# Kernel optimization log

Measured on AMD Instinct MI355X. Metric: run time of the kernel, lower is better.

The kernel has to match this reference:

```python
import jax, jax.numpy as jnp
import numpy as np

# Fixed per-step coefficients from the module __init__ (K = 16 steps)
_H = jnp.array([-0.73437643, 3.319645, 2.1290164, 3.6901689, 3.302721, 3.2154958,
                2.9151256, 3.1718695, 3.1084518, 2.6179547, 2.235003, 1.2864777,
                0.52327204, -0.08344932, -1.8249638, 3.0859442], dtype=jnp.float32)
_D = jnp.array([3.3848417, -0.07072583, 3.691287, 3.3074934, 3.2120926, 2.9196491,
                3.1727686, 3.1054153, 2.621943, 2.2355895, 1.2878408, 0.52468026,
                0.12632068, 0.14482783, 0.3153498, 0.13054803], dtype=jnp.float32)
_T = jnp.array([3.1538513, -1.0211663, 1.3714716, 1.0718397, 1.0049332, 0.68078244,
                1.0151638, 0.8858697, 0.4037103, 0.01490025, -0.90781677, -1.6859558,
                -1.9241625, -2.0441303, 0.279356, 0.1315174], dtype=jnp.float32)


@jax.custom_vjp
def spike(v_scaled):
    # Heaviside forward with surrogate gradient (matches SpikeFunction)
    return (v_scaled > 0).astype(v_scaled.dtype)

def _spike_fwd(v_scaled):
    return spike(v_scaled), v_scaled

def _spike_bwd(v_scaled, g):
    surrogate = jnp.maximum(1.0 - jnp.abs(v_scaled), 0.0)
    return (g * surrogate,)

spike.defvjp(_spike_fwd, _spike_bwd)


def setup_inputs() -> dict:
    key = jax.random.key(0)
    x = jax.random.normal(key, (16, 4096, 1024), dtype=jnp.float32)
    return {"x": x}


def reference(x) -> jnp.ndarray:
    zeros = jnp.zeros_like(x)

    def step(carry, hdt):
        v, z, out = carry
        h_t, d_t, T_t = hdt
        v = v - z * h_t
        v_scaled = (v - T_t) / (jnp.abs(v) + 1.0)
        z = spike(v_scaled)
        out = out + z * d_t
        return (v, z, out), None

    (_, _, out), _ = jax.lax.scan(step, (x, zeros, zeros), (_H, _D, _T))
    return out
```

## Files before the change

kernel.cpp:

```cpp
#include <hip/hip_runtime.h>


typedef float f32x4 __attribute__((ext_vector_type(4)));

__device__ __constant__ const float kH[16] = {
    -0.73437643f, 3.319645f,   2.1290164f,  3.6901689f,
    3.302721f,    3.2154958f,  2.9151256f,  3.1718695f,
    3.1084518f,   2.6179547f,  2.235003f,   1.2864777f,
    0.52327204f, -0.08344932f, -1.8249638f, 3.0859442f};

__device__ __constant__ const float kD[16] = {
    3.3848417f, -0.07072583f, 3.691287f,   3.3074934f,
    3.2120926f,  2.9196491f,  3.1727686f,  3.1054153f,
    2.621943f,   2.2355895f,  1.2878408f,  0.52468026f,
    0.12632068f, 0.14482783f, 0.3153498f,  0.13054803f};

__device__ __constant__ const float kT[16] = {
    3.1538513f, -1.0211663f,  1.3714716f,  1.0718397f,
    1.0049332f,  0.68078244f, 1.0151638f,  0.8858697f,
    0.4037103f,  0.01490025f, -0.90781677f, -1.6859558f,
    -1.9241625f, -2.0441303f, 0.279356f,   0.1315174f};

__device__ __forceinline__ float spike_chain(float v) {
    float z = (v > kT[0]) ? 1.0f : 0.0f;
    float out = z * kD[0];
#pragma unroll
    for (int t = 1; t < 16; ++t) {
        v = fmaf(-z, kH[t], v);
        z = (v > kT[t]) ? 1.0f : 0.0f;
        out = fmaf(z, kD[t], out);
    }
    return out;
}

__device__ __forceinline__ f32x4 spike4(f32x4 v) {
    f32x4 o;
    o.x = spike_chain(v.x);
    o.y = spike_chain(v.y);
    o.z = spike_chain(v.z);
    o.w = spike_chain(v.w);
    return o;
}

__global__ __launch_bounds__(256) void spike_kernel(const f32x4* __restrict__ x,
                                                    f32x4* __restrict__ out,
                                                    int n4) {
    const int T = gridDim.x * blockDim.x;
    int i = blockIdx.x * blockDim.x + threadIdx.x;

    for (; i + 3 * T < n4; i += 4 * T) {
        f32x4 a = x[i];
        f32x4 b = x[i + T];
        f32x4 c = x[i + 2 * T];
        f32x4 d = x[i + 3 * T];
        f32x4 ra = spike4(a);
        f32x4 rb = spike4(b);
        f32x4 rc = spike4(c);
        f32x4 rd = spike4(d);
        __builtin_nontemporal_store(ra, &out[i]);
        __builtin_nontemporal_store(rb, &out[i + T]);
        __builtin_nontemporal_store(rc, &out[i + 2 * T]);
        __builtin_nontemporal_store(rd, &out[i + 3 * T]);
    }
    for (; i < n4; i += T) {
        f32x4 r = spike4(x[i]);
        __builtin_nontemporal_store(r, &out[i]);
    }
}

extern "C" void kernel_launch(void* const* d_in, const int* in_sizes, int n_in,
                              void* d_out, int out_size, void* d_ws, size_t ws_size,
                              hipStream_t stream) {
    const float* x = (const float*)d_in[0];
    float* out = (float*)d_out;
    int n = in_sizes[0];
    int n4 = n >> 2;

    const int block = 256;
    int grid = (n4 + 4 * block - 1) / (4 * block);

    spike_kernel<<<grid, block, 0, stream>>>(
        (const f32x4*)x, (f32x4*)out, n4);
}
```

Before: 97.50 us.

## Replace spike compare-select with packed FMA clamp step function

Computes the spike indicator as clamp(v*BIG - T*BIG) using v_pk_fma_f32 with the clamp modifier, so each step becomes three packed FMAs over pairs of elements instead of a compare plus select plus scalar FMAs. The fixed-size path drops the loop and tail checks, and a generic fallback kernel handles other sizes. The clamp trick differs from an exact Heaviside when v is within about 1/BIG of the threshold, where it gives a fractional spike value, and that error can propagate through later steps.

```diff
diff --git a/kernel.cpp b/kernel.cpp
--- a/kernel.cpp
+++ b/kernel.cpp
@@ -1,25 +1,92 @@
 #include <hip/hip_runtime.h>
 
 
+typedef float f32x2 __attribute__((ext_vector_type(2)));
 typedef float f32x4 __attribute__((ext_vector_type(4)));
 
-__device__ __constant__ const float kH[16] = {
+static constexpr float kBIG = 1099511627776.0f;
+
+static constexpr float kH[16] = {
     -0.73437643f, 3.319645f,   2.1290164f,  3.6901689f,
     3.302721f,    3.2154958f,  2.9151256f,  3.1718695f,
     3.1084518f,   2.6179547f,  2.235003f,   1.2864777f,
     0.52327204f, -0.08344932f, -1.8249638f, 3.0859442f};
 
-__device__ __constant__ const float kD[16] = {
+static constexpr float kD[16] = {
     3.3848417f, -0.07072583f, 3.691287f,   3.3074934f,
     3.2120926f,  2.9196491f,  3.1727686f,  3.1054153f,
     2.621943f,   2.2355895f,  1.2878408f,  0.52468026f,
     0.12632068f, 0.14482783f, 0.3153498f,  0.13054803f};
 
-__device__ __constant__ const float kT[16] = {
+static constexpr float kT[16] = {
     3.1538513f, -1.0211663f,  1.3714716f,  1.0718397f,
     1.0049332f,  0.68078244f, 1.0151638f,  0.8858697f,
     0.4037103f,  0.01490025f, -0.90781677f, -1.6859558f,
     -1.9241625f, -2.0441303f, 0.279356f,   0.1315174f};
+
+__device__ __forceinline__ f32x2 pk_fma(f32x2 a, f32x2 b, f32x2 c) {
+    f32x2 d;
+    asm("v_pk_fma_f32 %0, %1, %2, %3" : "=v"(d) : "v"(a), "v"(b), "v"(c));
+    return d;
+}
+
+__device__ __forceinline__ f32x2 pk_fma_clamp(f32x2 a, f32x2 b, f32x2 c) {
+    f32x2 d;
+    asm("v_pk_fma_f32 %0, %1, %2, %3 clamp" : "=v"(d) : "v"(a), "v"(b), "v"(c));
+    return d;
+}
+
+__device__ __forceinline__ void spike8(f32x2 v[8], f32x2 o[8]) {
+    const f32x2 big = {kBIG, kBIG};
+    f32x2 z[8];
+    {
+        const f32x2 ts = {-kT[0] * kBIG, -kT[0] * kBIG};
+        const f32x2 dd = {kD[0], kD[0]};
+        const f32x2 zz = {0.0f, 0.0f};
+#pragma unroll
+        for (int c = 0; c < 8; ++c) {
+            z[c] = pk_fma_clamp(v[c], big, ts);
+            o[c] = pk_fma(z[c], dd, zz);
+        }
+    }
+#pragma unroll
+    for (int t = 1; t < 16; ++t) {
+        const f32x2 nh = {-kH[t], -kH[t]};
+        const f32x2 ts = {-kT[t] * kBIG, -kT[t] * kBIG};
+        const f32x2 dd = {kD[t], kD[t]};
+#pragma unroll
+        for (int c = 0; c < 8; ++c) {
+            v[c] = pk_fma(z[c], nh, v[c]);
+            z[c] = pk_fma_clamp(v[c], big, ts);
+            o[c] = pk_fma(z[c], dd, o[c]);
+        }
+    }
+}
+
+__global__ __launch_bounds__(256) void spike_kernel(const f32x4* __restrict__ x,
+                                                    f32x4* __restrict__ out) {
+    const int T = gridDim.x * blockDim.x;
+    const int i = blockIdx.x * blockDim.x + threadIdx.x;
+
+    f32x4 a0 = x[i];
+    f32x4 a1 = x[i + T];
+    f32x4 a2 = x[i + 2 * T];
+    f32x4 a3 = x[i + 3 * T];
+
+    f32x2 v[8] = {a0.xy, a0.zw, a1.xy, a1.zw, a2.xy, a2.zw, a3.xy, a3.zw};
+    f32x2 o[8];
+    spike8(v, o);
+
+    f32x4 r0 = {o[0].x, o[0].y, o[1].x, o[1].y};
+    f32x4 r1 = {o[2].x, o[2].y, o[3].x, o[3].y};
+    f32x4 r2 = {o[4].x, o[4].y, o[5].x, o[5].y};
+    f32x4 r3 = {o[6].x, o[6].y, o[7].x, o[7].y};
+
+    __builtin_nontemporal_store(r0, &out[i]);
+    __builtin_nontemporal_store(r1, &out[i + T]);
+    __builtin_nontemporal_store(r2, &out[i + 2 * T]);
+    __builtin_nontemporal_store(r3, &out[i + 3 * T]);
+}
 
 __device__ __forceinline__ float spike_chain(float v) {
     float z = (v > kT[0]) ? 1.0f : 0.0f;
@@ -33,37 +100,18 @@
     return out;
 }
 
-__device__ __forceinline__ f32x4 spike4(f32x4 v) {
-    f32x4 o;
-    o.x = spike_chain(v.x);
-    o.y = spike_chain(v.y);
-    o.z = spike_chain(v.z);
-    o.w = spike_chain(v.w);
-    return o;
-}
-
-__global__ __launch_bounds__(256) void spike_kernel(const f32x4* __restrict__ x,
-                                                    f32x4* __restrict__ out,
-                                                    int n4) {
+__global__ __launch_bounds__(256) void spike_generic(const f32x4* __restrict__ x,
+                                                     f32x4* __restrict__ out,
+                                                     int n4) {
     const int T = gridDim.x * blockDim.x;
     int i = blockIdx.x * blockDim.x + threadIdx.x;
-
-    for (; i + 3 * T < n4; i += 4 * T) {
+    for (; i < n4; i += T) {
         f32x4 a = x[i];
-        f32x4 b = x[i + T];
-        f32x4 c = x[i + 2 * T];
-        f32x4 d = x[i + 3 * T];
-        f32x4 ra = spike4(a);
-        f32x4 rb = spike4(b);
-        f32x4 rc = spike4(c);
-        f32x4 rd = spike4(d);
-        __builtin_nontemporal_store(ra, &out[i]);
-        __builtin_nontemporal_store(rb, &out[i + T]);
-        __builtin_nontemporal_store(rc, &out[i + 2 * T]);
-        __builtin_nontemporal_store(rd, &out[i + 3 * T]);
-    }
-    for (; i < n4; i += T) {
-        f32x4 r = spike4(x[i]);
+        f32x4 r;
+        r.x = spike_chain(a.x);
+        r.y = spike_chain(a.y);
+        r.z = spike_chain(a.z);
+        r.w = spike_chain(a.w);
         __builtin_nontemporal_store(r, &out[i]);
     }
 }
@@ -77,8 +125,16 @@
     int n4 = n >> 2;
 
     const int block = 256;
-    int grid = (n4 + 4 * block - 1) / (4 * block);
+    const int per_thread = 4;
 
-    spike_kernel<<<grid, block, 0, stream>>>(
-        (const f32x4*)x, (f32x4*)out, n4);
+    if (n4 % (block * per_thread) == 0) {
+        int grid = n4 / (block * per_thread);
+        spike_kernel<<<grid, block, 0, stream>>>(
+            (const f32x4*)x, (f32x4*)out);
+    } else {
+        int grid = (n4 + block - 1) / block;
+        if (grid > 4096) grid = 4096;
+        spike_generic<<<grid, block, 0, stream>>>(
+            (const f32x4*)x, (f32x4*)out, n4);
+    }
 }
```

Result: faster. 83.64 us (-14.2%).
